# Optimization experiments

Measured on AMD Instinct MI355X. Metric: run time of the kernel, lower is better.

## Reference

```python
import jax, jax.numpy as jnp
import numpy as np

B, N, J, D, H = 64, 128, 512, 1024, 4096
ITERS, EPS = 3, 1e-8
SCALE = D ** -0.5
LN_EPS = 1e-5  # torch LayerNorm default


def _ln(x, g, b):
    m = jnp.mean(x, axis=-1, keepdims=True)
    v = jnp.mean((x - m) ** 2, axis=-1, keepdims=True)
    return (x - m) * jax.lax.rsqrt(v + LN_EPS) * g + b


def setup_inputs() -> dict:
    key = jax.random.key(0)
    ks = jax.random.split(key, 24)
    p = lambda i, shape: jax.random.normal(ks[i], shape, jnp.float32) * 0.02
    return {
        "inputs": jax.random.normal(ks[0], (B, N, D), jnp.float32),
        "texts": jax.random.normal(ks[1], (J, D), jnp.float32),
        "Wq": p(2, (D, D)), "bq": jnp.zeros((D,), jnp.float32),
        "Wk": p(3, (D, D)), "bk": jnp.zeros((D,), jnp.float32),
        "Wv": p(4, (D, D)), "bv": jnp.zeros((D,), jnp.float32),
        "W_ih": p(5, (3 * D, D)), "b_ih": jnp.zeros((3 * D,), jnp.float32),
        "W_hh": p(6, (3 * D, D)), "b_hh": jnp.zeros((3 * D,), jnp.float32),
        "W1": p(7, (H, D)), "b1": jnp.zeros((H,), jnp.float32),
        "W2": p(8, (D, H)), "b2": jnp.zeros((D,), jnp.float32),
        "g_in": jnp.ones((D,), jnp.float32), "be_in": jnp.zeros((D,), jnp.float32),
        "g_sl": jnp.ones((D,), jnp.float32), "be_sl": jnp.zeros((D,), jnp.float32),
        "g_ff": jnp.ones((D,), jnp.float32), "be_ff": jnp.zeros((D,), jnp.float32),
    }


def reference(inputs, texts, Wq, bq, Wk, bk, Wv, bv, W_ih, b_ih, W_hh, b_hh,
              W1, b1, W2, b2, g_in, be_in, g_sl, be_sl, g_ff, be_ff):
    slots = inputs                                  # [B, N, D]
    texts_n = _ln(texts, g_in, be_in)               # [J, D] (repeat == broadcast)
    k = texts_n @ Wk.T + bk                         # [J, D]
    v = texts_n @ Wv.T + bv                         # [J, D]
    for _ in range(ITERS):
        slots_prev = slots
        q = _ln(slots, g_sl, be_sl) @ Wq.T + bq     # [B, N, D]
        dots = jnp.einsum('bid,jd->bij', q, k) * SCALE
        attn = jax.nn.softmax(dots, axis=1) + EPS   # softmax over slots dim
        attn = attn / jnp.sum(attn, axis=-1, keepdims=True)
        updates = jnp.einsum('jd,bij->bid', v, attn)
        # GRUCell: input=updates, hidden=slots_prev (torch gate order r, z, n)
        gi = updates @ W_ih.T + b_ih
        gh = slots_prev @ W_hh.T + b_hh
        i_r, i_z, i_n = jnp.split(gi, 3, axis=-1)
        h_r, h_z, h_n = jnp.split(gh, 3, axis=-1)
        r = jax.nn.sigmoid(i_r + h_r)
        z = jax.nn.sigmoid(i_z + h_z)
        n = jnp.tanh(i_n + r * h_n)
        slots = (1.0 - z) * n + z * slots_prev
        ff = _ln(slots, g_ff, be_ff)
        slots = slots + (jax.nn.relu(ff @ W1.T + b1) @ W2.T + b2)
    return slots
```

## Files before the change

### kernel.cpp

```cpp
#include <hip/hip_runtime.h>
#include <hip/hip_bf16.h>
#include <stdint.h>


using bf16 = __hip_bfloat16;
typedef __bf16 bf16x8 __attribute__((ext_vector_type(8)));
typedef float f32x4 __attribute__((ext_vector_type(4)));

#define F_RELU    1
#define F_SIGMOID 2
#define F_GRU     4
#define F_EPSC    8

__device__ __forceinline__ void gl_to_lds16(const void* g, void* l) {
  __builtin_amdgcn_global_load_lds(
      (const __attribute__((address_space(1))) uint32_t*)(uintptr_t)g,
      (__attribute__((address_space(3))) uint32_t*)(uintptr_t)l,
      16, 0, 0);
}

template <int BN>
__global__ __launch_bounds__(256, 4) void gemm_bt(
    const bf16* __restrict__ X, int ldx,
    const bf16* __restrict__ W, int ldw,
    const float* __restrict__ bias,
    int M, int N, int K, float scale, int flags,
    float* __restrict__ outF, int ldf,
    bf16* __restrict__ outB, int ldb,
    const float* __restrict__ resid,
    const bf16* __restrict__ rz,
    const bf16* __restrict__ hn,
    const float* __restrict__ auxA,
    const float* __restrict__ auxB)
{
  constexpr int NJ = BN / 32;
  __shared__ __align__(16) bf16 As[128 * 32];
  __shared__ __align__(16) bf16 Bs[BN * 32];
  const int t = threadIdx.x;
  const int m0 = blockIdx.x * 128, n0 = blockIdx.y * BN;
  const int wave = t >> 6, lane = t & 63;
  const int wm = (wave >> 1) * 64, wn = (wave & 1) * (BN / 2);
  const int lrow = lane & 15, quad = lane >> 4;

  f32x4 acc[4][NJ] = {};

  const int srow = t >> 2;
  const int scol = (t & 3) * 8;
  const bf16* Ag  = X + (size_t)(m0 + srow) * ldx + scol;
  const bf16* Ag2 = Ag + (size_t)64 * ldx;
  const bf16* Bg  = W + (size_t)(n0 + srow) * ldw + scol;
  const bf16* Bg2 = Bg + (size_t)64 * ldw;
  bf16* Al  = As + t * 8;
  bf16* Al2 = Al + 64 * 32;
  bf16* Bl  = Bs + t * 8;
  bf16* Bl2 = Bl + 64 * 32;

  for (int k0 = 0; k0 < K; k0 += 32) {
    gl_to_lds16(Ag + k0, Al);
    gl_to_lds16(Ag2 + k0, Al2);
    gl_to_lds16(Bg + k0, Bl);
    if (BN == 128) gl_to_lds16(Bg2 + k0, Bl2);
    __syncthreads();
    bf16x8 af[4], bfr[NJ];
    const bf16x8* Asv = (const bf16x8*)As;
    const bf16x8* Bsv = (const bf16x8*)Bs;
#pragma unroll
    for (int i = 0; i < 4; i++)  af[i]  = Asv[(wm + i * 16 + lrow) * 4 + quad];
#pragma unroll
    for (int j = 0; j < NJ; j++) bfr[j] = Bsv[(wn + j * 16 + lrow) * 4 + quad];
#pragma unroll
    for (int i = 0; i < 4; i++)
#pragma unroll
      for (int j = 0; j < NJ; j++)
        acc[i][j] = __builtin_amdgcn_mfma_f32_16x16x32_bf16(af[i], bfr[j], acc[i][j], 0, 0, 0);
    __syncthreads();
  }

#pragma unroll
  for (int i = 0; i < 4; i++) {
    const int row0 = m0 + wm + i * 16 + quad * 4;
#pragma unroll
    for (int j = 0; j < NJ; j++) {
      const int col = n0 + wn + j * 16 + lrow;
      const float badd = bias ? bias[col] : 0.f;
#pragma unroll
      for (int r = 0; r < 4; r++) {
        const int row = row0 + r;
        float val = acc[i][j][r] * scale + badd;
        if (flags & F_EPSC)    val += 1e-8f * auxA[col] * auxB[row];
        if (flags & F_RELU)    val = fmaxf(val, 0.f);
        if (flags & F_SIGMOID) val = 1.f / (1.f + expf(-val));
        if (flags & F_GRU) {
          const size_t ridx = (size_t)row * 1024 + col;
          const float rg = __bfloat162float(rz[(size_t)row * 2048 + col]);
          const float zg = __bfloat162float(rz[(size_t)row * 2048 + 1024 + col]);
          const float hv = __bfloat162float(hn[ridx]);
          const float ng = tanhf(val + rg * hv);
          const float prev = resid[ridx];
          val = (1.f - zg) * ng + zg * prev;
        } else if (resid) {
          val += resid[(size_t)row * ldf + col];
        }
        if (outF) outF[(size_t)row * ldf + col] = val;
        if (outB) outB[(size_t)row * ldb + col] = __float2bfloat16(val);
      }
    }
  }
}

__global__ __launch_bounds__(256) void ln_rows(const float* __restrict__ x,
    const float* __restrict__ g, const float* __restrict__ b,
    bf16* __restrict__ out, int ldo)
{
  const int row = blockIdx.x;
  const int t = threadIdx.x;
  const float* xr = x + (size_t)row * 1024;
  float v[4];
  float s = 0.f, s2 = 0.f;
#pragma unroll
  for (int i = 0; i < 4; i++) {
    float val = xr[t + 256 * i];
    v[i] = val; s += val; s2 += val * val;
  }
#pragma unroll
  for (int off = 32; off > 0; off >>= 1) {
    s  += __shfl_down(s, off);
    s2 += __shfl_down(s2, off);
  }
  __shared__ float rs[4], rs2[4];
  if ((t & 63) == 0) { rs[t >> 6] = s; rs2[t >> 6] = s2; }
  __syncthreads();
  const float S  = rs[0] + rs[1] + rs[2] + rs[3];
  const float S2 = rs2[0] + rs2[1] + rs2[2] + rs2[3];
  const float mean = S * (1.f / 1024.f);
  const float var  = S2 * (1.f / 1024.f) - mean * mean;
  const float rstd = rsqrtf(var + 1e-5f);
  bf16* outr = out + (size_t)row * ldo;
#pragma unroll
  for (int i = 0; i < 4; i++) {
    const int c = t + 256 * i;
    outr[c] = __float2bfloat16((v[i] - mean) * rstd * g[c] + b[c]);
  }
}

__global__ __launch_bounds__(256) void softmax_fused(
    const float* __restrict__ dots, bf16* __restrict__ xcat2,
    float* __restrict__ P)
{
  __shared__ float tile[128][65];
  __shared__ float cred[4][64];
  __shared__ float colmax[64], colinv[64];
  const int b = blockIdx.x, jt = blockIdx.y;
  const int t = threadIdx.x;
  const float* src = dots + (size_t)b * (128 * 512) + jt * 64;
#pragma unroll
  for (int p = 0; p < 32; p++) {
    const int i = p * 4 + (t >> 6), c = t & 63;
    tile[i][c] = src[(size_t)i * 512 + c];
  }
  __syncthreads();
  const int c = t & 63, s = t >> 6;
  float mx = -1e30f;
  for (int i = s * 32; i < s * 32 + 32; i++) mx = fmaxf(mx, tile[i][c]);
  cred[s][c] = mx;
  __syncthreads();
  if (s == 0) colmax[c] = fmaxf(fmaxf(cred[0][c], cred[1][c]),
                                fmaxf(cred[2][c], cred[3][c]));
  __syncthreads();
  const float cm = colmax[c];
  float sum = 0.f;
  for (int i = s * 32; i < s * 32 + 32; i++) {
    const float e = expf(tile[i][c] - cm);
    tile[i][c] = e; sum += e;
  }
  cred[s][c] = sum;
  __syncthreads();
  if (s == 0) colinv[c] = 1.f / (cred[0][c] + cred[1][c] + cred[2][c] + cred[3][c]);
  __syncthreads();
  bf16* dst = xcat2 + (size_t)b * 128 * 1536 + jt * 64;
#pragma unroll
  for (int p = 0; p < 32; p++) {
    const int i = p * 4 + (t >> 6), cc = t & 63;
    dst[(size_t)i * 1536 + cc] = __float2bfloat16(tile[i][cc] * colinv[cc]);
  }
  if (t < 128) {
    float rs = 0.f;
    for (int cc = 0; cc < 64; cc++) rs += tile[t][cc] * colinv[cc];
    P[((size_t)b * 128 + t) * 8 + jt] = rs;
  }
}

__global__ __launch_bounds__(256) void rowinv_k(const float* __restrict__ P,
                                                float* __restrict__ rowinv)
{
  const int m = blockIdx.x * 256 + threadIdx.x;
  const float* p = P + (size_t)m * 8;
  float s = 0.f;
#pragma unroll
  for (int i = 0; i < 8; i++) s += p[i];
  rowinv[m] = 1.f / (s + 512.f * 1e-8f);
}

__global__ __launch_bounds__(256) void smscale(bf16* __restrict__ x,
                                               const float* __restrict__ rinv)
{
  const int idx = blockIdx.x * 256 + threadIdx.x;
  const int m = idx >> 9, j = idx & 511;
  const size_t a = (size_t)m * 1536 + j;
  x[a] = __float2bfloat16(__bfloat162float(x[a]) * rinv[m]);
}

__global__ __launch_bounds__(256) void init_slots(const float* __restrict__ x,
    float* __restrict__ sf, bf16* __restrict__ xr)
{
  const size_t base = (size_t)blockIdx.x * 1024 + threadIdx.x;
#pragma unroll
  for (int i = 0; i < 4; i++) {
    const size_t idx = base + 256 * i;
    const float v = x[idx];
    sf[idx] = v;
    xr[(idx >> 10) * 1536 + (idx & 1023)] = __float2bfloat16(v);
  }
}

__global__ __launch_bounds__(256) void f2b(const float* __restrict__ x,
                                           bf16* __restrict__ y)
{
  const size_t base = (size_t)blockIdx.x * 1024 + threadIdx.x;
#pragma unroll
  for (int i = 0; i < 4; i++) y[base + 256 * i] = __float2bfloat16(x[base + 256 * i]);
}

__global__ __launch_bounds__(256) void f2b_ld(const float* __restrict__ src,
                                              bf16* __restrict__ dst, int dstld)
{
  const int idx = blockIdx.x * 256 + threadIdx.x;
  const int n = idx >> 10, c = idx & 1023;
  dst[(size_t)n * dstld + c] = __float2bfloat16(src[(size_t)n * 1024 + c]);
}

__global__ __launch_bounds__(256) void f2b_T(const float* __restrict__ Wq,
                                             bf16* __restrict__ wqT)
{
  const int idx = blockIdx.x * 256 + threadIdx.x;
  const int d = idx >> 10, dp = idx & 1023;
  wqT[idx] = __float2bfloat16(Wq[(size_t)dp * 1024 + d]);
}

__global__ __launch_bounds__(256) void make_brz(const float* __restrict__ bih,
    const float* __restrict__ bhh, float* __restrict__ brz)
{
  const int n = blockIdx.x * 256 + threadIdx.x;
  brz[n] = bih[n] + bhh[n];
}

__global__ __launch_bounds__(256) void make_bqk(const bf16* __restrict__ k,
    const float* __restrict__ bq, float* __restrict__ bqk, float scale)
{
  const int j = blockIdx.x * 256 + threadIdx.x;
  const bf16* kr = k + (size_t)j * 1024;
  float s = 0.f;
  for (int d = 0; d < 1024; d++) s += bq[d] * __bfloat162float(kr[d]);
  bqk[j] = scale * s;
}

__global__ __launch_bounds__(256) void make_vcol(const bf16* __restrict__ v,
                                                 float* __restrict__ vcol)
{
  const int d = blockIdx.x * 256 + threadIdx.x;
  float s = 0.f;
  for (int j = 0; j < 512; j++) s += __bfloat162float(v[(size_t)j * 1024 + d]);
  vcol[d] = s;
}

__global__ __launch_bounds__(256) void make_c(const float* __restrict__ Wih,
    const float* __restrict__ vcol, float* __restrict__ c)
{
  const int n = blockIdx.x;
  const int t = threadIdx.x;
  const float* wr = Wih + (size_t)n * 1024;
  float s = 0.f;
#pragma unroll
  for (int i = 0; i < 4; i++) s += wr[t + 256 * i] * vcol[t + 256 * i];
#pragma unroll
  for (int off = 32; off > 0; off >>= 1) s += __shfl_down(s, off);
  __shared__ float rs[4];
  if ((t & 63) == 0) rs[t >> 6] = s;
  __syncthreads();
  if (t == 0) c[n] = rs[0] + rs[1] + rs[2] + rs[3];
}

extern "C" void kernel_launch(void* const* d_in, const int* in_sizes, int n_in,
                              void* d_out, int out_size, void* d_ws, size_t ws_size,
                              hipStream_t stream)
{
  const float* inputs = (const float*)d_in[0];
  const float* texts  = (const float*)d_in[1];
  const float* Wq  = (const float*)d_in[2];  const float* bq  = (const float*)d_in[3];
  const float* Wk  = (const float*)d_in[4];  const float* bk  = (const float*)d_in[5];
  const float* Wv  = (const float*)d_in[6];  const float* bv  = (const float*)d_in[7];
  const float* Wih = (const float*)d_in[8];  const float* bih = (const float*)d_in[9];
  const float* Whh = (const float*)d_in[10]; const float* bhh = (const float*)d_in[11];
  const float* W1  = (const float*)d_in[12]; const float* b1  = (const float*)d_in[13];
  const float* W2  = (const float*)d_in[14]; const float* b2  = (const float*)d_in[15];
  const float* g_in = (const float*)d_in[16]; const float* be_in = (const float*)d_in[17];
  const float* g_sl = (const float*)d_in[18]; const float* be_sl = (const float*)d_in[19];
  const float* g_ff = (const float*)d_in[20]; const float* be_ff = (const float*)d_in[21];

  constexpr int B = 64, N = 128, J = 512, D = 1024, H = 4096;
  constexpr int M = B * N;
  const float SCALE = 0.03125f;

  char* ws = (char*)d_ws;
  size_t off = 0;
  auto alloc = [&](size_t bytes) -> char* {
    char* p = ws + off; off += (bytes + 255) & ~(size_t)255; return p;
  };
  bf16* wk_b    = (bf16*)alloc((size_t)D * D * 2);
  bf16* wv_b    = (bf16*)alloc((size_t)D * D * 2);
  bf16* w1_b    = (bf16*)alloc((size_t)H * D * 2);
  bf16* w2_b    = (bf16*)alloc((size_t)D * H * 2);
  bf16* whn_b   = (bf16*)alloc((size_t)D * D * 2);
  bf16* win_b   = (bf16*)alloc((size_t)D * D * 2);
  bf16* wihrz_b = (bf16*)alloc((size_t)2048 * D * 2);
  bf16* wqT_b   = (bf16*)alloc((size_t)D * D * 2);
  bf16* wcat2_b = (bf16*)alloc((size_t)2048 * 1536 * 2);
  bf16* ptn_b   = (bf16*)alloc((size_t)D * J * 2);
  bf16* kq_b    = (bf16*)alloc((size_t)J * D * 2);
  bf16* texts_n = (bf16*)alloc((size_t)J * D * 2);
  bf16* k_b     = (bf16*)alloc((size_t)J * D * 2);
  bf16* v_b     = (bf16*)alloc((size_t)J * D * 2);
  bf16* xcat2_b = (bf16*)alloc((size_t)M * 1536 * 2);
  float* brz_b  = (float*)alloc((size_t)2048 * 4);
  float* bqk_b  = (float*)alloc((size_t)J * 4);
  float* vcol_b = (float*)alloc((size_t)D * 4);
  float* c_b    = (float*)alloc((size_t)3072 * 4);
  float* P_b    = (float*)alloc((size_t)M * 8 * 4);
  float* rinv_b = (float*)alloc((size_t)M * 4);
  char* U = alloc((size_t)48 * 1024 * 1024);
  bf16*  xln_b  = (bf16*)(U);
  float* dots_f = (float*)(U + (size_t)16 * 1024 * 1024);
  bf16*  rz_b   = (bf16*)(U);
  bf16*  hn_b   = (bf16*)(U + (size_t)32 * 1024 * 1024);
  bf16*  h1_b   = (bf16*)(U + (size_t)16 * 1024 * 1024);

  if (ws_size < off) return;

  float* slots_f = (float*)d_out;

  f2b<<<dim3(D * D / 1024), 256, 0, stream>>>(Wk, wk_b);
  f2b<<<dim3(D * D / 1024), 256, 0, stream>>>(Wv, wv_b);
  f2b<<<dim3(H * D / 1024), 256, 0, stream>>>(W1, w1_b);
  f2b<<<dim3(D * H / 1024), 256, 0, stream>>>(W2, w2_b);
  f2b<<<dim3(D * D / 1024), 256, 0, stream>>>(Whh + (size_t)2048 * D, whn_b);
  f2b<<<dim3(D * D / 1024), 256, 0, stream>>>(Wih + (size_t)2048 * D, win_b);
  f2b<<<dim3(2048 * D / 1024), 256, 0, stream>>>(Wih, wihrz_b);
  f2b_T<<<dim3(D * D / 256), 256, 0, stream>>>(Wq, wqT_b);
  f2b_ld<<<dim3(2048 * 1024 / 256), 256, 0, stream>>>(Whh, wcat2_b + 512, 1536);
  make_brz<<<dim3(8), 256, 0, stream>>>(bih, bhh, brz_b);

  init_slots<<<dim3(M * D / 1024), 256, 0, stream>>>(inputs, slots_f, xcat2_b + 512);

  ln_rows<<<dim3(J), 256, 0, stream>>>(texts, g_in, be_in, texts_n, D);
  gemm_bt<64><<<dim3(J / 128, D / 64), 256, 0, stream>>>(
      texts_n, D, wk_b, D, bk, J, D, D, 1.f, 0,
      nullptr, 0, k_b, D, nullptr, nullptr, nullptr, nullptr, nullptr);
  gemm_bt<64><<<dim3(J / 128, D / 64), 256, 0, stream>>>(
      texts_n, D, wv_b, D, bv, J, D, D, 1.f, 0,
      nullptr, 0, v_b, D, nullptr, nullptr, nullptr, nullptr, nullptr);
  gemm_bt<64><<<dim3(J / 128, D / 64), 256, 0, stream>>>(
      k_b, D, wqT_b, D, nullptr, J, D, D, 1.f, 0,
      nullptr, 0, kq_b, D, nullptr, nullptr, nullptr, nullptr, nullptr);
  gemm_bt<64><<<dim3(2048 / 128, J / 64), 256, 0, stream>>>(
      wihrz_b, D, v_b, D, nullptr, 2048, J, D, 1.f, 0,
      nullptr, 0, wcat2_b, 1536, nullptr, nullptr, nullptr, nullptr, nullptr);
  gemm_bt<64><<<dim3(D / 128, J / 64), 256, 0, stream>>>(
      win_b, D, v_b, D, nullptr, D, J, D, 1.f, 0,
      nullptr, 0, ptn_b, J, nullptr, nullptr, nullptr, nullptr, nullptr);
  make_bqk<<<dim3(2), 256, 0, stream>>>(k_b, bq, bqk_b, SCALE);
  make_vcol<<<dim3(4), 256, 0, stream>>>(v_b, vcol_b);
  make_c<<<dim3(3072), 256, 0, stream>>>(Wih, vcol_b, c_b);

  for (int it = 0; it < 3; it++) {
    ln_rows<<<dim3(M), 256, 0, stream>>>(slots_f, g_sl, be_sl, xln_b, D);
    gemm_bt<64><<<dim3(M / 128, J / 64), 256, 0, stream>>>(
        xln_b, D, kq_b, D, bqk_b, M, J, D, SCALE, 0,
        dots_f, J, nullptr, 0, nullptr, nullptr, nullptr, nullptr, nullptr);
    softmax_fused<<<dim3(B, 8), 256, 0, stream>>>(dots_f, xcat2_b, P_b);
    rowinv_k<<<dim3(M / 256), 256, 0, stream>>>(P_b, rinv_b);
    smscale<<<dim3(M * 512 / 256), 256, 0, stream>>>(xcat2_b, rinv_b);
    gemm_bt<64><<<dim3(M / 128, D / 64), 256, 0, stream>>>(
        xcat2_b + 512, 1536, whn_b, D, bhh + 2048, M, D, D, 1.f, 0,
        nullptr, 0, hn_b, D, nullptr, nullptr, nullptr, nullptr, nullptr);
    gemm_bt<128><<<dim3(M / 128, 2048 / 128), 256, 0, stream>>>(
        xcat2_b, 1536, wcat2_b, 1536, brz_b, M, 2048, 1536, 1.f, F_SIGMOID | F_EPSC,
        nullptr, 0, rz_b, 2048, nullptr, nullptr, nullptr, c_b, rinv_b);
    gemm_bt<64><<<dim3(M / 128, D / 64), 256, 0, stream>>>(
        xcat2_b, 1536, ptn_b, J, bih + 2048, M, D, J, 1.f, F_GRU | F_EPSC,
        slots_f, D, xcat2_b + 512, 1536, slots_f, rz_b, hn_b, c_b + 2048, rinv_b);
    ln_rows<<<dim3(M), 256, 0, stream>>>(slots_f, g_ff, be_ff, xln_b, D);
    gemm_bt<128><<<dim3(M / 128, 2048 / 128), 256, 0, stream>>>(
        xln_b, D, w1_b, D, b1, M, 2048, D, 1.f, F_RELU,
        nullptr, 0, h1_b, 2048, nullptr, nullptr, nullptr, nullptr, nullptr);
    gemm_bt<64><<<dim3(M / 128, D / 64), 256, 0, stream>>>(
        h1_b, 2048, w2_b, H, b2, M, D, 2048, 1.f, 0,
        slots_f, D, nullptr, 0, slots_f, nullptr, nullptr, nullptr, nullptr);
    gemm_bt<128><<<dim3(M / 128, 2048 / 128), 256, 0, stream>>>(
        xln_b, D, w1_b + (size_t)2048 * D, D, b1 + 2048, M, 2048, D, 1.f, F_RELU,
        nullptr, 0, h1_b, 2048, nullptr, nullptr, nullptr, nullptr, nullptr);
    gemm_bt<64><<<dim3(M / 128, D / 64), 256, 0, stream>>>(
        h1_b, 2048, w2_b + 2048, H, nullptr, M, D, 2048, 1.f, 0,
        slots_f, D, xcat2_b + 512, 1536, slots_f, nullptr, nullptr, nullptr, nullptr);
  }
}
```

Baseline: 1.648 ms.

## Rewrite GEMM with 256-wide tiles, 512 threads and double-buffered LDS prefetch

The bf16 MFMA GEMM moves from 128xBN tiles with 256 threads and a single LDS buffer to BMx256 tiles with 512 threads (8 waves). It double-buffers LDS so the next K-slice is staged while MFMAs run on the current one. It also uses a column-chunked LDS layout and raises wave priority around the MFMA blocks. The aim is to hide global-load latency and raise data reuse per tile. In exchange it uses more LDS and registers per block and launches fewer blocks, which may underfill the CUs on the smaller GEMMs.

```diff
diff --git a/kernel.cpp b/kernel.cpp
--- a/kernel.cpp
+++ b/kernel.cpp
@@ -19,8 +19,8 @@
       16, 0, 0);
 }
 
-template <int BN>
-__global__ __launch_bounds__(256, 4) void gemm_bt(
+template <int BM>
+__global__ __launch_bounds__(512, 2) void gemm_bt(
     const bf16* __restrict__ X, int ldx,
     const bf16* __restrict__ W, int ldw,
     const float* __restrict__ bias,
@@ -33,60 +33,103 @@
     const float* __restrict__ auxA,
     const float* __restrict__ auxB)
 {
-  constexpr int NJ = BN / 32;
-  __shared__ __align__(16) bf16 As[128 * 32];
-  __shared__ __align__(16) bf16 Bs[BN * 32];
+  constexpr int MI = BM / 32;
+  constexpr int ABYTES = BM * 64;
+  constexpr int BUFB = ABYTES + 16384;
+  __shared__ __align__(16) char smem[2 * BUFB];
   const int t = threadIdx.x;
-  const int m0 = blockIdx.x * 128, n0 = blockIdx.y * BN;
-  const int wave = t >> 6, lane = t & 63;
-  const int wm = (wave >> 1) * 64, wn = (wave & 1) * (BN / 2);
+  const int m0 = blockIdx.x * BM, n0 = blockIdx.y * 256;
+  const int lane = t & 63, wave = t >> 6;
+  const int wm = wave >> 2, wn = wave & 3;
   const int lrow = lane & 15, quad = lane >> 4;
 
-  f32x4 acc[4][NJ] = {};
-
-  const int srow = t >> 2;
-  const int scol = (t & 3) * 8;
-  const bf16* Ag  = X + (size_t)(m0 + srow) * ldx + scol;
-  const bf16* Ag2 = Ag + (size_t)64 * ldx;
-  const bf16* Bg  = W + (size_t)(n0 + srow) * ldw + scol;
-  const bf16* Bg2 = Bg + (size_t)64 * ldw;
-  bf16* Al  = As + t * 8;
-  bf16* Al2 = Al + 64 * 32;
-  bf16* Bl  = Bs + t * 8;
-  bf16* Bl2 = Bl + 64 * 32;
-
-  for (int k0 = 0; k0 < K; k0 += 32) {
-    gl_to_lds16(Ag + k0, Al);
-    gl_to_lds16(Ag2 + k0, Al2);
-    gl_to_lds16(Bg + k0, Bl);
-    if (BN == 128) gl_to_lds16(Bg2 + k0, Bl2);
-    __syncthreads();
-    bf16x8 af[4], bfr[NJ];
-    const bf16x8* Asv = (const bf16x8*)As;
-    const bf16x8* Bsv = (const bf16x8*)Bs;
-#pragma unroll
-    for (int i = 0; i < 4; i++)  af[i]  = Asv[(wm + i * 16 + lrow) * 4 + quad];
-#pragma unroll
-    for (int j = 0; j < NJ; j++) bfr[j] = Bsv[(wn + j * 16 + lrow) * 4 + quad];
-#pragma unroll
-    for (int i = 0; i < 4; i++)
-#pragma unroll
-      for (int j = 0; j < NJ; j++)
-        acc[i][j] = __builtin_amdgcn_mfma_f32_16x16x32_bf16(af[i], bfr[j], acc[i][j], 0, 0, 0);
-    __syncthreads();
-  }
-
-#pragma unroll
-  for (int i = 0; i < 4; i++) {
-    const int row0 = m0 + wm + i * 16 + quad * 4;
-#pragma unroll
-    for (int j = 0; j < NJ; j++) {
-      const int col = n0 + wn + j * 16 + lrow;
+  f32x4 acc[MI][4] = {};
+  const int nt = K >> 5;
+
+  auto stage = [&](int wb, int k0) {
+    char* base = smem + wb * BUFB;
+    if constexpr (BM == 256) {
+#pragma unroll
+      for (int u = 0; u < 2; ++u) {
+        const int s = t + u * 512, c = s >> 8, r = s & 255;
+        gl_to_lds16(X + (size_t)(m0 + r) * ldx + k0 + c * 8,
+                    base + c * (BM * 16) + r * 16);
+      }
+    } else {
+      const int c = t >> 7, r = t & 127;
+      gl_to_lds16(X + (size_t)(m0 + r) * ldx + k0 + c * 8,
+                  base + c * (BM * 16) + r * 16);
+    }
+#pragma unroll
+    for (int u = 0; u < 2; ++u) {
+      const int s = t + u * 512, c = s >> 8, r = s & 255;
+      gl_to_lds16(W + (size_t)(n0 + r) * ldw + k0 + c * 8,
+                  base + ABYTES + c * 4096 + r * 16);
+    }
+  };
+
+  stage(0, 0);
+  asm volatile("s_waitcnt vmcnt(0)" ::: "memory");
+  __builtin_amdgcn_s_barrier();
+  asm volatile("" ::: "memory");
+
+  for (int tt = 0; tt < nt; ++tt) {
+    const int rbuf = tt & 1;
+    const bool pf = (tt + 1 < nt);
+    const bf16x8* AS = (const bf16x8*)(smem + rbuf * BUFB);
+    const bf16x8* BS = (const bf16x8*)(smem + rbuf * BUFB + ABYTES);
+    const int ab = quad * BM + wm * (BM / 2) + lrow;
+    const int bb = quad * 256 + wn * 64 + lrow;
+
+    bf16x8 af[4], bfr[4];
+#pragma unroll
+    for (int i = 0; i < 4; ++i) af[i] = AS[ab + i * 16];
+#pragma unroll
+    for (int j = 0; j < 4; ++j) bfr[j] = BS[bb + j * 16];
+    if (pf) stage(rbuf ^ 1, (tt + 1) << 5);
+    __builtin_amdgcn_s_barrier();
+    asm volatile("" ::: "memory");
+    __builtin_amdgcn_s_setprio(1);
+#pragma unroll
+    for (int i = 0; i < 4; ++i)
+#pragma unroll
+      for (int j = 0; j < 4; ++j)
+        acc[i][j] = __builtin_amdgcn_mfma_f32_16x16x32_bf16(
+            af[i], bfr[j], acc[i][j], 0, 0, 0);
+    __builtin_amdgcn_s_setprio(0);
+    if constexpr (BM == 256) {
+      __builtin_amdgcn_s_barrier();
+      asm volatile("" ::: "memory");
+      bf16x8 af2[4];
+#pragma unroll
+      for (int i = 0; i < 4; ++i) af2[i] = AS[ab + (4 + i) * 16];
+      __builtin_amdgcn_s_barrier();
+      asm volatile("" ::: "memory");
+      __builtin_amdgcn_s_setprio(1);
+#pragma unroll
+      for (int i = 0; i < 4; ++i)
+#pragma unroll
+        for (int j = 0; j < 4; ++j)
+          acc[4 + i][j] = __builtin_amdgcn_mfma_f32_16x16x32_bf16(
+              af2[i], bfr[j], acc[4 + i][j], 0, 0, 0);
+      __builtin_amdgcn_s_setprio(0);
+    }
+    asm volatile("s_waitcnt vmcnt(0) lgkmcnt(0)" ::: "memory");
+    __builtin_amdgcn_s_barrier();
+    asm volatile("" ::: "memory");
+  }
+
+#pragma unroll
+  for (int mi = 0; mi < MI; ++mi) {
+    const int row0 = m0 + wm * (BM / 2) + mi * 16 + quad * 4;
+#pragma unroll
+    for (int j = 0; j < 4; ++j) {
+      const int col = n0 + wn * 64 + j * 16 + lrow;
       const float badd = bias ? bias[col] : 0.f;
 #pragma unroll
       for (int r = 0; r < 4; r++) {
         const int row = row0 + r;
-        float val = acc[i][j][r] * scale + badd;
+        float val = acc[mi][j][r] * scale + badd;
         if (flags & F_EPSC)    val += 1e-8f * auxA[col] * auxB[row];
         if (flags & F_RELU)    val = fmaxf(val, 0.f);
         if (flags & F_SIGMOID) val = 1.f / (1.f + expf(-val));
@@ -362,19 +405,19 @@
   init_slots<<<dim3(M * D / 1024), 256, 0, stream>>>(inputs, slots_f, xcat2_b + 512);
 
   ln_rows<<<dim3(J), 256, 0, stream>>>(texts, g_in, be_in, texts_n, D);
-  gemm_bt<64><<<dim3(J / 128, D / 64), 256, 0, stream>>>(
+  gemm_bt<128><<<dim3(J / 128, D / 256), 512, 0, stream>>>(
       texts_n, D, wk_b, D, bk, J, D, D, 1.f, 0,
       nullptr, 0, k_b, D, nullptr, nullptr, nullptr, nullptr, nullptr);
-  gemm_bt<64><<<dim3(J / 128, D / 64), 256, 0, stream>>>(
+  gemm_bt<128><<<dim3(J / 128, D / 256), 512, 0, stream>>>(
       texts_n, D, wv_b, D, bv, J, D, D, 1.f, 0,
       nullptr, 0, v_b, D, nullptr, nullptr, nullptr, nullptr, nullptr);
-  gemm_bt<64><<<dim3(J / 128, D / 64), 256, 0, stream>>>(
+  gemm_bt<128><<<dim3(J / 128, D / 256), 512, 0, stream>>>(
       k_b, D, wqT_b, D, nullptr, J, D, D, 1.f, 0,
       nullptr, 0, kq_b, D, nullptr, nullptr, nullptr, nullptr, nullptr);
-  gemm_bt<64><<<dim3(2048 / 128, J / 64), 256, 0, stream>>>(
+  gemm_bt<128><<<dim3(2048 / 128, J / 256), 512, 0, stream>>>(
       wihrz_b, D, v_b, D, nullptr, 2048, J, D, 1.f, 0,
       nullptr, 0, wcat2_b, 1536, nullptr, nullptr, nullptr, nullptr, nullptr);
-  gemm_bt<64><<<dim3(D / 128, J / 64), 256, 0, stream>>>(
+  gemm_bt<128><<<dim3(D / 128, J / 256), 512, 0, stream>>>(
       win_b, D, v_b, D, nullptr, D, J, D, 1.f, 0,
       nullptr, 0, ptn_b, J, nullptr, nullptr, nullptr, nullptr, nullptr);
   make_bqk<<<dim3(2), 256, 0, stream>>>(k_b, bq, bqk_b, SCALE);
@@ -383,32 +426,32 @@
 
   for (int it = 0; it < 3; it++) {
     ln_rows<<<dim3(M), 256, 0, stream>>>(slots_f, g_sl, be_sl, xln_b, D);
-    gemm_bt<64><<<dim3(M / 128, J / 64), 256, 0, stream>>>(
+    gemm_bt<128><<<dim3(M / 128, J / 256), 512, 0, stream>>>(
         xln_b, D, kq_b, D, bqk_b, M, J, D, SCALE, 0,
         dots_f, J, nullptr, 0, nullptr, nullptr, nullptr, nullptr, nullptr);
     softmax_fused<<<dim3(B, 8), 256, 0, stream>>>(dots_f, xcat2_b, P_b);
     rowinv_k<<<dim3(M / 256), 256, 0, stream>>>(P_b, rinv_b);
     smscale<<<dim3(M * 512 / 256), 256, 0, stream>>>(xcat2_b, rinv_b);
-    gemm_bt<64><<<dim3(M / 128, D / 64), 256, 0, stream>>>(
+    gemm_bt<128><<<dim3(M / 128, D / 256), 512, 0, stream>>>(
         xcat2_b + 512, 1536, whn_b, D, bhh + 2048, M, D, D, 1.f, 0,
         nullptr, 0, hn_b, D, nullptr, nullptr, nullptr, nullptr, nullptr);
-    gemm_bt<128><<<dim3(M / 128, 2048 / 128), 256, 0, stream>>>(
+    gemm_bt<256><<<dim3(M / 256, 2048 / 256), 512, 0, stream>>>(
         xcat2_b, 1536, wcat2_b, 1536, brz_b, M, 2048, 1536, 1.f, F_SIGMOID | F_EPSC,
         nullptr, 0, rz_b, 2048, nullptr, nullptr, nullptr, c_b, rinv_b);
-    gemm_bt<64><<<dim3(M / 128, D / 64), 256, 0, stream>>>(
+    gemm_bt<128><<<dim3(M / 128, D / 256), 512, 0, stream>>>(
         xcat2_b, 1536, ptn_b, J, bih + 2048, M, D, J, 1.f, F_GRU | F_EPSC,
         slots_f, D, xcat2_b + 512, 1536, slots_f, rz_b, hn_b, c_b + 2048, rinv_b);
     ln_rows<<<dim3(M), 256, 0, stream>>>(slots_f, g_ff, be_ff, xln_b, D);
-    gemm_bt<128><<<dim3(M / 128, 2048 / 128), 256, 0, stream>>>(
+    gemm_bt<256><<<dim3(M / 256, 2048 / 256), 512, 0, stream>>>(
         xln_b, D, w1_b, D, b1, M, 2048, D, 1.f, F_RELU,
         nullptr, 0, h1_b, 2048, nullptr, nullptr, nullptr, nullptr, nullptr);
-    gemm_bt<64><<<dim3(M / 128, D / 64), 256, 0, stream>>>(
+    gemm_bt<128><<<dim3(M / 128, D / 256), 512, 0, stream>>>(
         h1_b, 2048, w2_b, H, b2, M, D, 2048, 1.f, 0,
         slots_f, D, nullptr, 0, slots_f, nullptr, nullptr, nullptr, nullptr);
-    gemm_bt<128><<<dim3(M / 128, 2048 / 128), 256, 0, stream>>>(
+    gemm_bt<256><<<dim3(M / 256, 2048 / 256), 512, 0, stream>>>(
         xln_b, D, w1_b + (size_t)2048 * D, D, b1 + 2048, M, 2048, D, 1.f, F_RELU,
         nullptr, 0, h1_b, 2048, nullptr, nullptr, nullptr, nullptr, nullptr);
-    gemm_bt<64><<<dim3(M / 128, D / 64), 256, 0, stream>>>(
+    gemm_bt<128><<<dim3(M / 128, D / 256), 512, 0, stream>>>(
         h1_b, 2048, w2_b + 2048, H, nullptr, M, D, 2048, 1.f, 0,
         slots_f, D, xcat2_b + 512, 1536, slots_f, nullptr, nullptr, nullptr, nullptr);
   }
```

Result: slower. 2.664 ms (+61.7%).

## Double K-tile depth to 64 and XOR-swizzle LDS layout in GEMM

Applied to the files above, without the earlier changes.

The GEMM main loop now loads 64-wide K slices per iteration instead of 32, halving the number of barrier pairs per tile. Global-to-LDS loads are arranged with an XOR swizzle of the 16-byte column chunk by row, and fragment reads apply the matching swizzle to avoid LDS bank conflicts. The cost is doubled shared memory per block, which may reduce occupancy under the 4-blocks launch bound, and it requires K to be a multiple of 64.

```diff
diff --git a/kernel.cpp b/kernel.cpp
--- a/kernel.cpp
+++ b/kernel.cpp
@@ -34,8 +34,8 @@
     const float* __restrict__ auxB)
 {
   constexpr int NJ = BN / 32;
-  __shared__ __align__(16) bf16 As[128 * 32];
-  __shared__ __align__(16) bf16 Bs[BN * 32];
+  __shared__ __align__(16) bf16 As[128 * 64];
+  __shared__ __align__(16) bf16 Bs[BN * 64];
   const int t = threadIdx.x;
   const int m0 = blockIdx.x * 128, n0 = blockIdx.y * BN;
   const int wave = t >> 6, lane = t & 63;
@@ -44,35 +44,41 @@
 
   f32x4 acc[4][NJ] = {};
 
-  const int srow = t >> 2;
-  const int scol = (t & 3) * 8;
-  const bf16* Ag  = X + (size_t)(m0 + srow) * ldx + scol;
-  const bf16* Ag2 = Ag + (size_t)64 * ldx;
-  const bf16* Bg  = W + (size_t)(n0 + srow) * ldw + scol;
-  const bf16* Bg2 = Bg + (size_t)64 * ldw;
-  bf16* Al  = As + t * 8;
-  bf16* Al2 = Al + 64 * 32;
-  bf16* Bl  = Bs + t * 8;
-  bf16* Bl2 = Bl + 64 * 32;
-
-  for (int k0 = 0; k0 < K; k0 += 32) {
-    gl_to_lds16(Ag + k0, Al);
-    gl_to_lds16(Ag2 + k0, Al2);
-    gl_to_lds16(Bg + k0, Bl);
-    if (BN == 128) gl_to_lds16(Bg2 + k0, Bl2);
+  const int srow = t >> 3;
+  const int scol = ((t & 7) ^ (srow & 7)) * 8;
+  const bf16* Ag = X + (size_t)(m0 + srow) * ldx + scol;
+  const bf16* Bg = W + (size_t)(n0 + srow) * ldw + scol;
+  bf16* Al = As + t * 8;
+  bf16* Bl = Bs + t * 8;
+
+  const int r3 = lrow & 7;
+  const int c0 = quad ^ r3;
+  const int c1 = (4 + quad) ^ r3;
+
+  for (int k0 = 0; k0 < K; k0 += 64) {
+#pragma unroll
+    for (int u = 0; u < 4; ++u)
+      gl_to_lds16(Ag + k0 + (size_t)(u * 32) * ldx, Al + u * 2048);
+#pragma unroll
+    for (int u = 0; u < NJ; ++u)
+      gl_to_lds16(Bg + k0 + (size_t)(u * 32) * ldw, Bl + u * 2048);
     __syncthreads();
-    bf16x8 af[4], bfr[NJ];
-    const bf16x8* Asv = (const bf16x8*)As;
-    const bf16x8* Bsv = (const bf16x8*)Bs;
-#pragma unroll
-    for (int i = 0; i < 4; i++)  af[i]  = Asv[(wm + i * 16 + lrow) * 4 + quad];
-#pragma unroll
-    for (int j = 0; j < NJ; j++) bfr[j] = Bsv[(wn + j * 16 + lrow) * 4 + quad];
-#pragma unroll
-    for (int i = 0; i < 4; i++)
-#pragma unroll
-      for (int j = 0; j < NJ; j++)
-        acc[i][j] = __builtin_amdgcn_mfma_f32_16x16x32_bf16(af[i], bfr[j], acc[i][j], 0, 0, 0);
+    const bf16x8* AS = (const bf16x8*)As;
+    const bf16x8* BS = (const bf16x8*)Bs;
+#pragma unroll
+    for (int kk = 0; kk < 2; ++kk) {
+      const int ck = kk ? c1 : c0;
+      bf16x8 af[4], bfr[NJ];
+#pragma unroll
+      for (int i = 0; i < 4; i++)  af[i]  = AS[(wm + i * 16 + lrow) * 8 + ck];
+#pragma unroll
+      for (int j = 0; j < NJ; j++) bfr[j] = BS[(wn + j * 16 + lrow) * 8 + ck];
+#pragma unroll
+      for (int i = 0; i < 4; i++)
+#pragma unroll
+        for (int j = 0; j < NJ; j++)
+          acc[i][j] = __builtin_amdgcn_mfma_f32_16x16x32_bf16(af[i], bfr[j], acc[i][j], 0, 0, 0);
+    }
     __syncthreads();
   }
 
```

After: 1.611 ms. 1.02x faster.
